# Optimization experiments

Measured on AMD Instinct MI355X. Metric: run time of the kernel, lower is better.

The kernel has to match this reference:

```python
import jax, jax.numpy as jnp
import numpy as np
import math

C = 256
GROUPS = 8
EPS = 1e-5


def setup_inputs() -> dict:
    key = jax.random.key(0)
    ks = jax.random.split(key, 12)
    b, c, h, w = 4, C, 64, 64
    s = 1.0 / math.sqrt(c)
    return {
        "x": jax.random.normal(ks[0], (b, c, h, w), dtype=jnp.float32),
        "gamma": jax.random.normal(ks[1], (c,), dtype=jnp.float32) * 0.1 + 1.0,
        "beta": jax.random.normal(ks[2], (c,), dtype=jnp.float32) * 0.1,
        "wq": jax.random.normal(ks[3], (c, c), dtype=jnp.float32) * s,
        "bq": jnp.zeros((c,), dtype=jnp.float32),
        "wk": jax.random.normal(ks[4], (c, c), dtype=jnp.float32) * s,
        "bk": jnp.zeros((c,), dtype=jnp.float32),
        "wv": jax.random.normal(ks[5], (c, c), dtype=jnp.float32) * s,
        "bv": jnp.zeros((c,), dtype=jnp.float32),
        "wp": jax.random.normal(ks[6], (c, c), dtype=jnp.float32) * s,
        "bp": jnp.zeros((c,), dtype=jnp.float32),
    }


def _group_norm(x, gamma, beta):
    b, c, h, w = x.shape
    xg = x.reshape(b, GROUPS, c // GROUPS, h * w)
    mean = xg.mean(axis=(2, 3), keepdims=True)
    var = xg.var(axis=(2, 3), keepdims=True)
    xn = ((xg - mean) * jax.lax.rsqrt(var + EPS)).reshape(b, c, h, w)
    return xn * gamma[None, :, None, None] + beta[None, :, None, None]


def _conv1x1(x, w, b):
    # 1x1 conv == per-pixel channel GEMM
    return jnp.einsum('oc,bchw->bohw', w, x) + b[None, :, None, None]


def reference(x, gamma, beta, wq, bq, wk, bk, wv, bv, wp, bp):
    b, c, h, w = x.shape
    n = h * w
    xn = _group_norm(x, gamma, beta)
    q = _conv1x1(xn, wq, bq).reshape(b, c, n)  # [b,c,n]
    k = _conv1x1(xn, wk, bk).reshape(b, c, n)
    v = _conv1x1(xn, wv, bv).reshape(b, c, n)
    scale = 1.0 / math.sqrt(c)
    scores = jnp.einsum('bcn,bcm->bnm', q, k) * scale  # [b,n,n]
    attn = jax.nn.softmax(scores, axis=-1)
    out = jnp.einsum('bnm,bcm->bcn', attn, v).reshape(b, c, h, w)
    return _conv1x1(out, wp, bp) + x
```

## Files before the change

### kernel.cpp

```cpp
#include <hip/hip_runtime.h>
#include <hip/hip_bf16.h>
#include <math.h>


#define CCH 256
#define NPIX 4096
#define NB 4
#define NG 8
#define EPS 1e-5f
#define NCHUNK 4

typedef __attribute__((ext_vector_type(8))) short short8;
typedef __attribute__((ext_vector_type(4))) short short4v;
typedef __attribute__((ext_vector_type(4))) float f32x4;
typedef __attribute__((ext_vector_type(16))) float f32x16;
typedef unsigned short ushort_t;
typedef unsigned char u8;

#define GLD16(g, l) __builtin_amdgcn_global_load_lds( \
    (const __attribute__((address_space(1))) unsigned int*)(g), \
    (__attribute__((address_space(3))) unsigned int*)(l), 16, 0, 0)

#define WAITV(n) asm volatile("s_waitcnt vmcnt(" #n ")" ::: "memory")

__device__ inline ushort_t f2bf(float x) {
    union { float f; unsigned u; } c; c.f = x;
    unsigned r = c.u + 0x7FFFu + ((c.u >> 16) & 1u);
    return (ushort_t)(r >> 16);
}
__device__ inline float bf2f(ushort_t h) {
    union { unsigned u; float f; } c; c.u = ((unsigned)h) << 16;
    return c.f;
}
__device__ inline u8 f2fp8(float x) {
    return (u8)(__builtin_amdgcn_cvt_pk_fp8_f32(x, x, 0, false) & 0xff);
}
__device__ inline long mk64(unsigned lo, unsigned hi) {
    return (long)(((unsigned long long)hi << 32) | lo);
}

__global__ __launch_bounds__(256) void gn1w(const float* __restrict__ x,
                                            const float* __restrict__ wq,
                                            const float* __restrict__ wk,
                                            const float* __restrict__ wv,
                                            const float* __restrict__ wp,
                                            float* __restrict__ part,
                                            ushort_t* __restrict__ wbf,
                                            ushort_t* __restrict__ wpbf) {
    int bid = blockIdx.x;
    int t = threadIdx.x;
    if (bid >= 256) {
        int widx = bid - 256;
        int wi = widx >> 6;
        const float* src = wi == 0 ? wq : wi == 1 ? wk : wi == 2 ? wv : wp;
        ushort_t* dst = wi == 3 ? wpbf : wbf + wi * 65536;
        int i = (widx & 63) * 1024 + t * 4;
        float4 v = *(const float4*)(src + i);
        short4v o;
        o[0] = (short)f2bf(v.x); o[1] = (short)f2bf(v.y);
        o[2] = (short)f2bf(v.z); o[3] = (short)f2bf(v.w);
        *(short4v*)(dst + i) = o;
        return;
    }
    int bg = bid >> 3;
    int slice = bid & 7;
    const float* base = x + (size_t)bg * 32 * NPIX + (size_t)slice * 16384;
    float s = 0.f, sq = 0.f;
    for (int i = t; i < 4096; i += 256) {
        float4 v = ((const float4*)base)[i];
        s  += v.x + v.y + v.z + v.w;
        sq += v.x*v.x + v.y*v.y + v.z*v.z + v.w*v.w;
    }
    for (int off = 32; off; off >>= 1) {
        s  += __shfl_down(s,  off);
        sq += __shfl_down(sq, off);
    }
    __shared__ float red[8];
    int wid = t >> 6;
    if ((t & 63) == 0) { red[wid*2] = s; red[wid*2+1] = sq; }
    __syncthreads();
    if (t == 0) {
        float ts = 0.f, tq = 0.f;
        for (int wv2 = 0; wv2 < 4; wv2++) { ts += red[wv2*2]; tq += red[wv2*2+1]; }
        part[bid*2] = ts; part[bid*2+1] = tq;
    }
}

__global__ __launch_bounds__(256) void gn_transpose(const float* __restrict__ x,
                                                    const float* __restrict__ part,
                                                    const float* __restrict__ gamma,
                                                    const float* __restrict__ beta,
                                                    ushort_t* __restrict__ xnT) {
    __shared__ float T[64][69];
    __shared__ float gmean[2], grstd[2];
    int t = threadIdx.x;
    int nBase = blockIdx.x * 64;
    int cBase = blockIdx.y * 64;
    int b = blockIdx.z;
    if (t < 2) {
        int g = (cBase >> 5) + t;
        float s = 0.f, sq = 0.f;
        for (int i = 0; i < 8; i++) {
            s  += part[((b*NG + g)*8 + i)*2];
            sq += part[((b*NG + g)*8 + i)*2 + 1];
        }
        const float inv = 1.f / 131072.f;
        float mean = s * inv;
        float var = sq * inv - mean * mean;
        gmean[t] = mean;
        grstd[t] = rsqrtf(var + EPS);
    }
    __syncthreads();
    const float* xb = x + (size_t)b * CCH * NPIX;
    int n4  = (t & 15) * 4;
    int cc0 = (t >> 4) * 4;
    for (int i = 0; i < 4; i++) {
        int cc = cc0 + i;
        int c = cBase + cc;
        int gi = cc >> 5;
        float ga = gamma[c] * grstd[gi];
        float be = beta[c] - gmean[gi] * ga;
        float4 v = *(const float4*)&xb[(size_t)c * NPIX + nBase + n4];
        T[cc][n4+0] = v.x * ga + be;
        T[cc][n4+1] = v.y * ga + be;
        T[cc][n4+2] = v.z * ga + be;
        T[cc][n4+3] = v.w * ga + be;
    }
    __syncthreads();
    int nn  = t >> 2;
    int ci0 = (t & 3) * 16;
    short8 o0, o1;
    for (int j = 0; j < 8; j++) {
        o0[j] = (short)f2bf(T[ci0 + j][nn]);
        o1[j] = (short)f2bf(T[ci0 + 8 + j][nn]);
    }
    ushort_t* dst = xnT + ((size_t)b * NPIX + nBase + nn) * CCH + cBase + ci0;
    *(short8*)dst = o0;
    *((short8*)dst + 1) = o1;
}

__global__ __launch_bounds__(256, 2) void qkv3(const ushort_t* __restrict__ xnT,
                                               const ushort_t* __restrict__ wbf,
                                               const float* __restrict__ bq,
                                               const float* __restrict__ bk,
                                               const float* __restrict__ bv,
                                               u8* __restrict__ qT,
                                               u8* __restrict__ kT,
                                               u8* __restrict__ vv) {
    __shared__ __align__(16) ushort_t As[2][4096];
    __shared__ __align__(16) ushort_t Bs[2][4096];
    int t = threadIdx.x;
    int w = t >> 6, l = t & 63, quad = l >> 4, l16 = l & 15;
    int z = blockIdx.z;
    const ushort_t* A; const ushort_t* B; int mBase, nBase;
    if (z < 2) { A = xnT; B = wbf + z * 65536; mBase = blockIdx.x * 128; nBase = blockIdx.y * 128; }
    else       { A = wbf + 131072; B = xnT;    mBase = blockIdx.y * 128; nBase = blockIdx.x * 128; }
    int m0 = (w & 1) * 64, n0 = (w >> 1) * 64;

    const f32x4 fz = {0.f, 0.f, 0.f, 0.f};
    f32x4 acc[4][4];
    #pragma unroll
    for (int i = 0; i < 4; i++)
        #pragma unroll
        for (int j = 0; j < 4; j++) acc[i][j] = fz;

    int srow = t >> 2;
    int slc  = (t & 3) ^ ((t >> 2) & 3);
    int sldso = (t >> 6) * 512;

    #pragma unroll
    for (int j = 0; j < 2; j++) {
        int row = 64*j + srow;
        GLD16(A + (size_t)(mBase + row) * 256 + slc * 8, &As[0][j*2048 + sldso]);
        GLD16(B + (size_t)(nBase + row) * 256 + slc * 8, &Bs[0][j*2048 + sldso]);
    }
    int buf = 0;
    for (int kb = 0; kb < 8; kb++) {
        __syncthreads();
        if (kb < 7) {
            #pragma unroll
            for (int j = 0; j < 2; j++) {
                int row = 64*j + srow;
                GLD16(A + (size_t)(mBase + row) * 256 + (kb+1)*32 + slc * 8, &As[buf^1][j*2048 + sldso]);
                GLD16(B + (size_t)(nBase + row) * 256 + (kb+1)*32 + slc * 8, &Bs[buf^1][j*2048 + sldso]);
            }
        }
        short8 af[4], bfr[4];
        #pragma unroll
        for (int mb = 0; mb < 4; mb++)
            af[mb] = *(short8*)&As[buf][(m0 + mb*16 + l16)*32 + ((quad ^ (l16 & 3)) * 8)];
        #pragma unroll
        for (int nb = 0; nb < 4; nb++)
            bfr[nb] = *(short8*)&Bs[buf][(n0 + nb*16 + l16)*32 + ((quad ^ (l16 & 3)) * 8)];
        #pragma unroll
        for (int mb = 0; mb < 4; mb++)
            #pragma unroll
            for (int nb = 0; nb < 4; nb++)
                acc[mb][nb] = __builtin_amdgcn_mfma_f32_16x16x32_bf16(af[mb], bfr[nb], acc[mb][nb], 0, 0, 0);
        buf ^= 1;
    }
    if (z < 2) {
        const float* bias = z ? bk : bq;
        u8* C = z ? kT : qT;
        #pragma unroll
        for (int nb = 0; nb < 4; nb++) {
            int n = nBase + n0 + nb*16 + l16;
            float bb = bias[n];
            #pragma unroll
            for (int mb = 0; mb < 4; mb++)
                #pragma unroll
                for (int r = 0; r < 4; r++) {
                    int m = mBase + m0 + mb*16 + quad*4 + r;
                    C[(size_t)m * 256 + n] = f2fp8(acc[mb][nb][r] + bb);
                }
        }
    } else {
        #pragma unroll
        for (int mb = 0; mb < 4; mb++)
            #pragma unroll
            for (int r = 0; r < 4; r++) {
                int m = mBase + m0 + mb*16 + quad*4 + r;
                float bb = bv[m];
                #pragma unroll
                for (int nb = 0; nb < 4; nb++) {
                    int n = nBase + n0 + nb*16 + l16;
                    vv[((size_t)(n >> 12) * 256 + m) * 4096 + (n & 4095)] = f2fp8(acc[mb][nb][r] + bb);
                }
            }
    }
}

__global__ __launch_bounds__(256, 2) void flash_attn(const u8* __restrict__ qT,
                                                     const u8* __restrict__ kT,
                                                     const u8* __restrict__ vv,
                                                     ushort_t* __restrict__ Op0,
                                                     ushort_t* __restrict__ Op1,
                                                     ushort_t* __restrict__ Op2,
                                                     ushort_t* __restrict__ Op3,
                                                     float* __restrict__ lsum) {
    __shared__ __align__(16) u8 KsAll[3 * 8192];
    __shared__ __align__(16) u8 VsAll[3 * 8192];
    int t = threadIdx.x;
    int w = t >> 6, l = t & 63;
    int l32 = l & 31, hl = l >> 5;
    int flat = blockIdx.x;
    int xcd = flat & 7;
    int ix = flat >> 3;
    int combo = xcd + 8 * (ix >> 5);
    int qg = ix & 31;
    int chunk = combo & 3, b = combo >> 2;
    int qw = qg * 128 + w * 32;

    long qf[16];
    {
        const u8* qrow = qT + ((size_t)b * NPIX + qw + l32) * 256 + hl * 8;
        #pragma unroll
        for (int cb = 0; cb < 16; cb++) qf[cb] = *(const long*)(qrow + cb * 16);
    }

    f32x16 accO[8];
    #pragma unroll
    for (int i = 0; i < 8; i++)
        #pragma unroll
        for (int r = 0; r < 16; r++) accO[i][r] = 0.f;
    float lqa = 0.f;

    const u8* kbase = kT + (size_t)b * NPIX * 256;
    const u8* vbase = vv + (size_t)b * 256 * NPIX;

    const float SC = 0.0625f * 1.44269504089f;
    int mStart = chunk * (NPIX / NCHUNK);
    const int NT = (NPIX / NCHUNK) / 32;

    const u8* kaddr[2];
    const u8* vaddr[2];
    #pragma unroll
    for (int j = 0; j < 2; j++) {
        int n = j * 256 + t;
        int kkv = n >> 4, kcb = (n & 15) ^ (kkv & 7);
        int vc = n >> 1,  vsw = (n & 1) ^ ((vc >> 2) & 1);
        kaddr[j] = kbase + (size_t)(mStart + kkv) * 256 + kcb * 16;
        vaddr[j] = vbase + (size_t)vc * NPIX + mStart + vsw * 16;
    }

    int kO[8];
    #pragma unroll
    for (int c = 0; c < 8; c++) kO[c] = l32 * 256 + ((c ^ (l32 & 7)) * 16) + hl * 8;
    int sw0 = (l32 >> 2) & 1;
    int vO0 = l32 * 32 + (sw0 ^ 0) * 16 + hl * 8;
    int vO1 = l32 * 32 + (sw0 ^ 1) * 16 + hl * 8;

#define LDK(c) (*(const long*)&KsAll[kO[(c) & 7] + (((c) & 8) << 4)])
#define LDV0(m) (*(const long*)&VsAll[vO0 + (m) * 1024])
#define LDV1(m) (*(const long*)&VsAll[vO1 + (m) * 1024])

#define KISSUE(tile, slot) { \
        unsigned koff_ = (unsigned)(tile) * 8192u; \
        _Pragma("unroll") \
        for (int j = 0; j < 2; j++) \
            GLD16(kaddr[j] + koff_, &KsAll[(slot)*8192 + (j*256 + t)*16]); }
#define VISSUE(tile, slot) { \
        unsigned voff_ = (unsigned)(tile) * 32u; \
        _Pragma("unroll") \
        for (int j = 0; j < 2; j++) \
            GLD16(vaddr[j] + voff_, &VsAll[(slot)*8192 + (j*256 + t)*16]); }

#define SOFTMAX_PACK() { \
        float p_[16]; float q0_ = 0.f, q1_ = 0.f; \
        _Pragma("unroll") \
        for (int r = 0; r < 16; r++) { \
            float pe_ = exp2f(fmaf(sTa[r], SC, -5.0f)); \
            pe_ = fminf(pe_, 240.f); \
            p_[r] = pe_; \
            if (r & 1) q1_ += pe_; else q0_ += pe_; \
        } \
        lqa += q0_ + q1_; \
        unsigned pk0_ = (unsigned)__builtin_amdgcn_cvt_pk_fp8_f32(p_[2], p_[3], \
                        __builtin_amdgcn_cvt_pk_fp8_f32(p_[0], p_[1], 0, false), true); \
        unsigned pk1_ = (unsigned)__builtin_amdgcn_cvt_pk_fp8_f32(p_[6], p_[7], \
                        __builtin_amdgcn_cvt_pk_fp8_f32(p_[4], p_[5], 0, false), true); \
        unsigned pk2_ = (unsigned)__builtin_amdgcn_cvt_pk_fp8_f32(p_[10], p_[11], \
                        __builtin_amdgcn_cvt_pk_fp8_f32(p_[8], p_[9], 0, false), true); \
        unsigned pk3_ = (unsigned)__builtin_amdgcn_cvt_pk_fp8_f32(p_[14], p_[15], \
                        __builtin_amdgcn_cvt_pk_fp8_f32(p_[12], p_[13], 0, false), true); \
        asm("v_permlane32_swap_b32 %0, %1" : "+v"(pk0_), "+v"(pk1_)); \
        asm("v_permlane32_swap_b32 %0, %1" : "+v"(pk2_), "+v"(pk3_)); \
        B0 = mk64(pk0_, pk1_); \
        B1 = mk64(pk2_, pk3_); }

#define BURST() { \
        _Pragma("unroll") \
        for (int r = 0; r < 16; r++) sTa[r] = 0.f; \
        _Pragma("unroll") \
        for (int m = 0; m < 8; m++) { \
            sTa = __builtin_amdgcn_mfma_f32_32x32x16_fp8_fp8(LDK(2*m), qf[2*m], sTa, 0, 0, 0); \
            accO[m] = __builtin_amdgcn_mfma_f32_32x32x16_fp8_fp8(LDV0(m), B0, accO[m], 0, 0, 0); \
            sTa = __builtin_amdgcn_mfma_f32_32x32x16_fp8_fp8(LDK(2*m+1), qf[2*m+1], sTa, 0, 0, 0); \
            accO[m] = __builtin_amdgcn_mfma_f32_32x32x16_fp8_fp8(LDV1(m), B1, accO[m], 0, 0, 0); \
        } }

    KISSUE(0, 0);
    VISSUE(0, 0);
    KISSUE(1, 1);
    WAITV(4);
    __builtin_amdgcn_s_barrier();

    f32x16 sTa;
    #pragma unroll
    for (int r = 0; r < 16; r++) sTa[r] = 0.f;
    #pragma unroll
    for (int cb = 0; cb < 16; cb++)
        sTa = __builtin_amdgcn_mfma_f32_32x32x16_fp8_fp8(LDK(cb), qf[cb], sTa, 0, 0, 0);
    long B0, B1;
    SOFTMAX_PACK();

    #pragma unroll
    for (int c = 0; c < 8; c++) kO[c] += 8192;

    int ks_r = 1, ks_w = 2, vs_r = 0, vs_w = 1;
    #pragma unroll 1
    for (int tt = 0; tt < NT - 2; ++tt) {
        KISSUE(tt + 2, ks_w);
        VISSUE(tt + 1, vs_w);
        WAITV(4);
        __builtin_amdgcn_s_barrier();
        __builtin_amdgcn_sched_barrier(0);
        __builtin_amdgcn_s_setprio(1);
        BURST();
        __builtin_amdgcn_s_setprio(0);
        SOFTMAX_PACK();
        int dK = (ks_r == 2) ? -16384 : 8192;
        int dV = (vs_r == 2) ? -16384 : 8192;
        #pragma unroll
        for (int c = 0; c < 8; c++) kO[c] += dK;
        vO0 += dV; vO1 += dV;
        ks_r = ks_r + 1; if (ks_r == 3) ks_r = 0;
        ks_w = ks_w + 1; if (ks_w == 3) ks_w = 0;
        vs_r = vs_r + 1; if (vs_r == 3) vs_r = 0;
        vs_w = vs_w + 1; if (vs_w == 3) vs_w = 0;
    }

    VISSUE(NT - 1, vs_w);
    WAITV(2);
    __builtin_amdgcn_s_barrier();
    __builtin_amdgcn_sched_barrier(0);
    __builtin_amdgcn_s_setprio(1);
    BURST();
    __builtin_amdgcn_s_setprio(0);
    SOFTMAX_PACK();
    {
        int dV = (vs_r == 2) ? -16384 : 8192;
        vO0 += dV; vO1 += dV;
        vs_r = vs_r + 1; if (vs_r == 3) vs_r = 0;
    }

    WAITV(0);
    __builtin_amdgcn_s_barrier();
    {
        __builtin_amdgcn_s_setprio(1);
        #pragma unroll
        for (int m = 0; m < 8; m++) {
            accO[m] = __builtin_amdgcn_mfma_f32_32x32x16_fp8_fp8(LDV0(m), B0, accO[m], 0, 0, 0);
            accO[m] = __builtin_amdgcn_mfma_f32_32x32x16_fp8_fp8(LDV1(m), B1, accO[m], 0, 0, 0);
        }
        __builtin_amdgcn_s_setprio(0);
    }

    {
        float v = lqa + __shfl_xor(lqa, 32);
        if (hl == 0)
            lsum[((size_t)chunk * NB + b) * NPIX + qw + l32] = v;
    }
    ushort_t* op = chunk == 0 ? Op0 : chunk == 1 ? Op1 : chunk == 2 ? Op2 : Op3;
    size_t rowb = ((size_t)b * NPIX + qw + l32) * CCH;
    #pragma unroll
    for (int cblk = 0; cblk < 8; cblk++)
        #pragma unroll
        for (int a = 0; a < 4; a++) {
            short4v o;
            #pragma unroll
            for (int r = 0; r < 4; r++) o[r] = (short)f2bf(accO[cblk][a*4 + r]);
            *(short4v*)&op[rowb + cblk*32 + a*8 + hl*4] = o;
        }
#undef LDK
#undef LDV0
#undef LDV1
#undef KISSUE
#undef VISSUE
#undef SOFTMAX_PACK
#undef BURST
}

__global__ __launch_bounds__(256) void attn_combine(ushort_t* __restrict__ Op0,
                                                    const ushort_t* __restrict__ Op1,
                                                    const ushort_t* __restrict__ Op2,
                                                    const ushort_t* __restrict__ Op3,
                                                    const float* __restrict__ lsum) {
    const size_t BN = (size_t)NB * NPIX;
    size_t base = ((size_t)blockIdx.x * 256 + threadIdx.x) * 4;
    size_t bn = base >> 8;
    float li = 1.f / (lsum[bn] + lsum[BN + bn] + lsum[2*BN + bn] + lsum[3*BN + bn]);
    short4v a0 = *(short4v*)&Op0[base];
    short4v a1 = *(const short4v*)&Op1[base];
    short4v a2 = *(const short4v*)&Op2[base];
    short4v a3 = *(const short4v*)&Op3[base];
    short4v o;
    #pragma unroll
    for (int i = 0; i < 4; i++) {
        float v = (bf2f((ushort_t)a0[i]) + bf2f((ushort_t)a1[i]) +
                   bf2f((ushort_t)a2[i]) + bf2f((ushort_t)a3[i])) * li;
        o[i] = (short)f2bf(v);
    }
    *(short4v*)&Op0[base] = o;
}

__global__ __launch_bounds__(256, 2) void projk(const ushort_t* __restrict__ wpbf,
                                                const ushort_t* __restrict__ aoT,
                                                const float* __restrict__ bp,
                                                const float* __restrict__ x,
                                                float* __restrict__ out) {
    __shared__ __align__(16) ushort_t As[2][4096];
    __shared__ __align__(16) ushort_t Bs[2][4096];
    int t = threadIdx.x;
    int w = t >> 6, l = t & 63, quad = l >> 4, l16 = l & 15;
    int mBase = blockIdx.y * 128, nBase = blockIdx.x * 128;
    int m0 = (w & 1) * 64, n0 = (w >> 1) * 64;

    const f32x4 fz = {0.f, 0.f, 0.f, 0.f};
    f32x4 acc[4][4];
    #pragma unroll
    for (int i = 0; i < 4; i++)
        #pragma unroll
        for (int j = 0; j < 4; j++) acc[i][j] = fz;

    int srow = t >> 2;
    int slc  = (t & 3) ^ ((t >> 2) & 3);
    int sldso = (t >> 6) * 512;

    #pragma unroll
    for (int j = 0; j < 2; j++) {
        int row = 64*j + srow;
        GLD16(wpbf + (size_t)(mBase + row) * 256 + slc * 8, &As[0][j*2048 + sldso]);
        GLD16(aoT  + (size_t)(nBase + row) * 256 + slc * 8, &Bs[0][j*2048 + sldso]);
    }
    int buf = 0;
    for (int kb = 0; kb < 8; kb++) {
        __syncthreads();
        if (kb < 7) {
            #pragma unroll
            for (int j = 0; j < 2; j++) {
                int row = 64*j + srow;
                GLD16(wpbf + (size_t)(mBase + row) * 256 + (kb+1)*32 + slc * 8, &As[buf^1][j*2048 + sldso]);
                GLD16(aoT  + (size_t)(nBase + row) * 256 + (kb+1)*32 + slc * 8, &Bs[buf^1][j*2048 + sldso]);
            }
        }
        short8 af[4], bfr[4];
        #pragma unroll
        for (int mb = 0; mb < 4; mb++)
            af[mb] = *(short8*)&As[buf][(m0 + mb*16 + l16)*32 + ((quad ^ (l16 & 3)) * 8)];
        #pragma unroll
        for (int nb = 0; nb < 4; nb++)
            bfr[nb] = *(short8*)&Bs[buf][(n0 + nb*16 + l16)*32 + ((quad ^ (l16 & 3)) * 8)];
        #pragma unroll
        for (int mb = 0; mb < 4; mb++)
            #pragma unroll
            for (int nb = 0; nb < 4; nb++)
                acc[mb][nb] = __builtin_amdgcn_mfma_f32_16x16x32_bf16(af[mb], bfr[nb], acc[mb][nb], 0, 0, 0);
        buf ^= 1;
    }
    #pragma unroll
    for (int mb = 0; mb < 4; mb++)
        #pragma unroll
        for (int r = 0; r < 4; r++) {
            int m = mBase + m0 + mb*16 + quad*4 + r;
            float bb = bp[m];
            #pragma unroll
            for (int nb = 0; nb < 4; nb++) {
                int n = nBase + n0 + nb*16 + l16;
                size_t idx = ((size_t)(n >> 12) * 256 + m) * 4096 + (n & 4095);
                out[idx] = acc[mb][nb][r] + bb + x[idx];
            }
        }
}

extern "C" void kernel_launch(void* const* d_in, const int* in_sizes, int n_in,
                              void* d_out, int out_size, void* d_ws, size_t ws_size,
                              hipStream_t stream) {
    const float* x     = (const float*)d_in[0];
    const float* gamma = (const float*)d_in[1];
    const float* beta  = (const float*)d_in[2];
    const float* wq    = (const float*)d_in[3];
    const float* bq    = (const float*)d_in[4];
    const float* wk    = (const float*)d_in[5];
    const float* bk    = (const float*)d_in[6];
    const float* wv    = (const float*)d_in[7];
    const float* bv    = (const float*)d_in[8];
    const float* wp    = (const float*)d_in[9];
    const float* bp    = (const float*)d_in[10];
    float* out = (float*)d_out;

    const size_t SZ = (size_t)NB * NPIX * CCH;
    float* part  = (float*)d_ws;
    float* lsum  = part + 512;
    ushort_t* wpbf = (ushort_t*)(lsum + (size_t)NCHUNK * NB * NPIX);
    ushort_t* slot0 = wpbf + 65536;
    ushort_t* Op3 = slot0;
    u8* qT8 = (u8*)(slot0 + SZ);
    u8* kT8 = (u8*)(slot0 + 2*SZ);
    u8* vv8 = (u8*)(slot0 + 3*SZ);
    ushort_t* aoT = slot0 + 4*SZ;
    ushort_t* xnT = (ushort_t*)d_out;
    ushort_t* Op1 = (ushort_t*)d_out;
    ushort_t* Op2 = (ushort_t*)d_out + SZ;
    ushort_t* wbf = (ushort_t*)d_out + SZ;

    gn1w<<<512, 256, 0, stream>>>(x, wq, wk, wv, wp, part, wbf, wpbf);
    gn_transpose<<<dim3(64, 4, 4), 256, 0, stream>>>(x, part, gamma, beta, xnT);
    qkv3<<<dim3(128, 2, 3), 256, 0, stream>>>(xnT, wbf, bq, bk, bv, qT8, kT8, vv8);
    flash_attn<<<dim3(512), 256, 0, stream>>>(qT8, kT8, vv8, aoT, Op1, Op2, Op3, lsum);
    attn_combine<<<(int)(SZ / 1024), 256, 0, stream>>>(aoT, Op1, Op2, Op3, lsum);
    projk<<<dim3(128, 2), 256, 0, stream>>>(wpbf, aoT, bp, x, out);
}
```

Baseline: 196.3 us.

## Use scaled 32x32x64 FP8 MFMA and batch PV over two key tiles

Replaces the 32x32x16 FP8 MFMAs in the flash-attention loop with the MX-scaled 32x32x64 f8f6f4 MFMA, using unit scales. The QK^T step now takes 4 instructions per tile instead of 16. PV is deferred so that one set of 8 wide MFMAs covers two consecutive 32-key tiles, with a permlane swap building the combined P operand. V gets a 4-slot LDS ring to keep two tiles resident, and the XOR swizzles on K and V are dropped. Risks are LDS bank conflicts from the unswizzled 32-byte reads, less interleaving of QK and PV work, and more LDS use, which may affect the 2-blocks-per-CU occupancy.

```diff
diff --git a/kernel.cpp b/kernel.cpp
--- a/kernel.cpp
+++ b/kernel.cpp
@@ -14,6 +14,8 @@
 typedef __attribute__((ext_vector_type(4))) short short4v;
 typedef __attribute__((ext_vector_type(4))) float f32x4;
 typedef __attribute__((ext_vector_type(16))) float f32x16;
+typedef __attribute__((ext_vector_type(4))) int i32x4;
+typedef __attribute__((ext_vector_type(8))) int i32x8;
 typedef unsigned short ushort_t;
 typedef unsigned char u8;
 
@@ -22,6 +24,9 @@
     (__attribute__((address_space(3))) unsigned int*)(l), 16, 0, 0)
 
 #define WAITV(n) asm volatile("s_waitcnt vmcnt(" #n ")" ::: "memory")
+
+#define MXMFMA(A, B, C) __builtin_amdgcn_mfma_scale_f32_32x32x64_f8f6f4( \
+    (A), (B), (C), 0, 0, 0, 0x7F7F7F7F, 0, 0x7F7F7F7F)
 
 __device__ inline ushort_t f2bf(float x) {
     union { float f; unsigned u; } c; c.f = x;
@@ -35,8 +40,13 @@
 __device__ inline u8 f2fp8(float x) {
     return (u8)(__builtin_amdgcn_cvt_pk_fp8_f32(x, x, 0, false) & 0xff);
 }
-__device__ inline long mk64(unsigned lo, unsigned hi) {
-    return (long)(((unsigned long long)hi << 32) | lo);
+__device__ inline i32x8 ld32(const u8* p) {
+    i32x4 a = *(const i32x4*)p;
+    i32x4 b = *(const i32x4*)(p + 16);
+    i32x8 r;
+    r[0] = a[0]; r[1] = a[1]; r[2] = a[2]; r[3] = a[3];
+    r[4] = b[0]; r[5] = b[1]; r[6] = b[2]; r[7] = b[3];
+    return r;
 }
 
 __global__ __launch_bounds__(256) void gn1w(const float* __restrict__ x,
@@ -239,7 +249,7 @@
                                                      ushort_t* __restrict__ Op3,
                                                      float* __restrict__ lsum) {
     __shared__ __align__(16) u8 KsAll[3 * 8192];
-    __shared__ __align__(16) u8 VsAll[3 * 8192];
+    __shared__ __align__(16) u8 VsAll[4 * 8192];
     int t = threadIdx.x;
     int w = t >> 6, l = t & 63;
     int l32 = l & 31, hl = l >> 5;
@@ -251,11 +261,11 @@
     int chunk = combo & 3, b = combo >> 2;
     int qw = qg * 128 + w * 32;
 
-    long qf[16];
+    i32x8 qf4[4];
     {
-        const u8* qrow = qT + ((size_t)b * NPIX + qw + l32) * 256 + hl * 8;
-        #pragma unroll
-        for (int cb = 0; cb < 16; cb++) qf[cb] = *(const long*)(qrow + cb * 16);
+        const u8* qrow = qT + ((size_t)b * NPIX + qw + l32) * 256 + hl * 32;
+        #pragma unroll
+        for (int i = 0; i < 4; i++) qf4[i] = ld32(qrow + i * 64);
     }
 
     f32x16 accO[8];
@@ -277,22 +287,9 @@
     #pragma unroll
     for (int j = 0; j < 2; j++) {
         int n = j * 256 + t;
-        int kkv = n >> 4, kcb = (n & 15) ^ (kkv & 7);
-        int vc = n >> 1,  vsw = (n & 1) ^ ((vc >> 2) & 1);
-        kaddr[j] = kbase + (size_t)(mStart + kkv) * 256 + kcb * 16;
-        vaddr[j] = vbase + (size_t)vc * NPIX + mStart + vsw * 16;
-    }
-
-    int kO[8];
-    #pragma unroll
-    for (int c = 0; c < 8; c++) kO[c] = l32 * 256 + ((c ^ (l32 & 7)) * 16) + hl * 8;
-    int sw0 = (l32 >> 2) & 1;
-    int vO0 = l32 * 32 + (sw0 ^ 0) * 16 + hl * 8;
-    int vO1 = l32 * 32 + (sw0 ^ 1) * 16 + hl * 8;
-
-#define LDK(c) (*(const long*)&KsAll[kO[(c) & 7] + (((c) & 8) << 4)])
-#define LDV0(m) (*(const long*)&VsAll[vO0 + (m) * 1024])
-#define LDV1(m) (*(const long*)&VsAll[vO1 + (m) * 1024])
+        kaddr[j] = kbase + (size_t)(mStart + (n >> 4)) * 256 + (n & 15) * 16;
+        vaddr[j] = vbase + (size_t)(n >> 1) * NPIX + mStart + (n & 1) * 16;
+    }
 
 #define KISSUE(tile, slot) { \
         unsigned koff_ = (unsigned)(tile) * 8192u; \
@@ -305,7 +302,16 @@
         for (int j = 0; j < 2; j++) \
             GLD16(vaddr[j] + voff_, &VsAll[(slot)*8192 + (j*256 + t)*16]); }
 
-#define SOFTMAX_PACK() { \
+#define SCOMPUTE(slot) { \
+        const u8* kb_ = &KsAll[(slot)*8192] + l32*256 + hl*32; \
+        _Pragma("unroll") \
+        for (int r = 0; r < 16; r++) sTa[r] = 0.f; \
+        sTa = MXMFMA(ld32(kb_),       qf4[0], sTa); \
+        sTa = MXMFMA(ld32(kb_ + 64),  qf4[1], sTa); \
+        sTa = MXMFMA(ld32(kb_ + 128), qf4[2], sTa); \
+        sTa = MXMFMA(ld32(kb_ + 192), qf4[3], sTa); }
+
+#define SOFTMAX_PK(dst) { \
         float p_[16]; float q0_ = 0.f, q1_ = 0.f; \
         _Pragma("unroll") \
         for (int r = 0; r < 16; r++) { \
@@ -315,96 +321,72 @@
             if (r & 1) q1_ += pe_; else q0_ += pe_; \
         } \
         lqa += q0_ + q1_; \
-        unsigned pk0_ = (unsigned)__builtin_amdgcn_cvt_pk_fp8_f32(p_[2], p_[3], \
-                        __builtin_amdgcn_cvt_pk_fp8_f32(p_[0], p_[1], 0, false), true); \
-        unsigned pk1_ = (unsigned)__builtin_amdgcn_cvt_pk_fp8_f32(p_[6], p_[7], \
-                        __builtin_amdgcn_cvt_pk_fp8_f32(p_[4], p_[5], 0, false), true); \
-        unsigned pk2_ = (unsigned)__builtin_amdgcn_cvt_pk_fp8_f32(p_[10], p_[11], \
-                        __builtin_amdgcn_cvt_pk_fp8_f32(p_[8], p_[9], 0, false), true); \
-        unsigned pk3_ = (unsigned)__builtin_amdgcn_cvt_pk_fp8_f32(p_[14], p_[15], \
-                        __builtin_amdgcn_cvt_pk_fp8_f32(p_[12], p_[13], 0, false), true); \
-        asm("v_permlane32_swap_b32 %0, %1" : "+v"(pk0_), "+v"(pk1_)); \
-        asm("v_permlane32_swap_b32 %0, %1" : "+v"(pk2_), "+v"(pk3_)); \
-        B0 = mk64(pk0_, pk1_); \
-        B1 = mk64(pk2_, pk3_); }
-
-#define BURST() { \
+        dst[0] = (unsigned)__builtin_amdgcn_cvt_pk_fp8_f32(p_[2], p_[3], \
+                 __builtin_amdgcn_cvt_pk_fp8_f32(p_[0], p_[1], 0, false), true); \
+        dst[1] = (unsigned)__builtin_amdgcn_cvt_pk_fp8_f32(p_[6], p_[7], \
+                 __builtin_amdgcn_cvt_pk_fp8_f32(p_[4], p_[5], 0, false), true); \
+        dst[2] = (unsigned)__builtin_amdgcn_cvt_pk_fp8_f32(p_[10], p_[11], \
+                 __builtin_amdgcn_cvt_pk_fp8_f32(p_[8], p_[9], 0, false), true); \
+        dst[3] = (unsigned)__builtin_amdgcn_cvt_pk_fp8_f32(p_[14], p_[15], \
+                 __builtin_amdgcn_cvt_pk_fp8_f32(p_[12], p_[13], 0, false), true); }
+
+#define OCOMPUTE(slotE, slotO) { \
+        asm("v_permlane32_swap_b32 %0, %1" : "+v"(pkA[0]), "+v"(pkB[0])); \
+        asm("v_permlane32_swap_b32 %0, %1" : "+v"(pkA[1]), "+v"(pkB[1])); \
+        asm("v_permlane32_swap_b32 %0, %1" : "+v"(pkA[2]), "+v"(pkB[2])); \
+        asm("v_permlane32_swap_b32 %0, %1" : "+v"(pkA[3]), "+v"(pkB[3])); \
+        i32x8 pb; \
+        pb[0] = (int)pkA[0]; pb[1] = (int)pkB[0]; \
+        pb[2] = (int)pkA[1]; pb[3] = (int)pkB[1]; \
+        pb[4] = (int)pkA[2]; pb[5] = (int)pkB[2]; \
+        pb[6] = (int)pkA[3]; pb[7] = (int)pkB[3]; \
+        const u8* vb_ = &VsAll[(hl ? (slotO) : (slotE)) * 8192] + l32*32; \
         _Pragma("unroll") \
-        for (int r = 0; r < 16; r++) sTa[r] = 0.f; \
-        _Pragma("unroll") \
-        for (int m = 0; m < 8; m++) { \
-            sTa = __builtin_amdgcn_mfma_f32_32x32x16_fp8_fp8(LDK(2*m), qf[2*m], sTa, 0, 0, 0); \
-            accO[m] = __builtin_amdgcn_mfma_f32_32x32x16_fp8_fp8(LDV0(m), B0, accO[m], 0, 0, 0); \
-            sTa = __builtin_amdgcn_mfma_f32_32x32x16_fp8_fp8(LDK(2*m+1), qf[2*m+1], sTa, 0, 0, 0); \
-            accO[m] = __builtin_amdgcn_mfma_f32_32x32x16_fp8_fp8(LDV1(m), B1, accO[m], 0, 0, 0); \
-        } }
+        for (int cblk = 0; cblk < 8; cblk++) \
+            accO[cblk] = MXMFMA(ld32(vb_ + cblk*1024), pb, accO[cblk]); }
 
     KISSUE(0, 0);
     VISSUE(0, 0);
     KISSUE(1, 1);
-    WAITV(4);
+    WAITV(2);
     __builtin_amdgcn_s_barrier();
 
     f32x16 sTa;
-    #pragma unroll
-    for (int r = 0; r < 16; r++) sTa[r] = 0.f;
-    #pragma unroll
-    for (int cb = 0; cb < 16; cb++)
-        sTa = __builtin_amdgcn_mfma_f32_32x32x16_fp8_fp8(LDK(cb), qf[cb], sTa, 0, 0, 0);
-    long B0, B1;
-    SOFTMAX_PACK();
-
-    #pragma unroll
-    for (int c = 0; c < 8; c++) kO[c] += 8192;
-
-    int ks_r = 1, ks_w = 2, vs_r = 0, vs_w = 1;
+    unsigned pkA[4], pkB[4];
+    SCOMPUTE(0);
+    SOFTMAX_PK(pkA);
+
+    int ks_r = 1, ks_w = 2;
     #pragma unroll 1
     for (int tt = 0; tt < NT - 2; ++tt) {
         KISSUE(tt + 2, ks_w);
-        VISSUE(tt + 1, vs_w);
+        VISSUE(tt + 1, (tt + 1) & 3);
         WAITV(4);
         __builtin_amdgcn_s_barrier();
         __builtin_amdgcn_sched_barrier(0);
         __builtin_amdgcn_s_setprio(1);
-        BURST();
+        if (tt & 1) { OCOMPUTE((tt - 1) & 3, tt & 3); }
+        SCOMPUTE(ks_r);
         __builtin_amdgcn_s_setprio(0);
-        SOFTMAX_PACK();
-        int dK = (ks_r == 2) ? -16384 : 8192;
-        int dV = (vs_r == 2) ? -16384 : 8192;
-        #pragma unroll
-        for (int c = 0; c < 8; c++) kO[c] += dK;
-        vO0 += dV; vO1 += dV;
+        if (tt & 1) { SOFTMAX_PK(pkA); } else { SOFTMAX_PK(pkB); }
         ks_r = ks_r + 1; if (ks_r == 3) ks_r = 0;
         ks_w = ks_w + 1; if (ks_w == 3) ks_w = 0;
-        vs_r = vs_r + 1; if (vs_r == 3) vs_r = 0;
-        vs_w = vs_w + 1; if (vs_w == 3) vs_w = 0;
-    }
-
-    VISSUE(NT - 1, vs_w);
+    }
+
+    VISSUE(NT - 1, (NT - 1) & 3);
     WAITV(2);
     __builtin_amdgcn_s_barrier();
     __builtin_amdgcn_sched_barrier(0);
     __builtin_amdgcn_s_setprio(1);
-    BURST();
+    SCOMPUTE(ks_r);
     __builtin_amdgcn_s_setprio(0);
-    SOFTMAX_PACK();
-    {
-        int dV = (vs_r == 2) ? -16384 : 8192;
-        vO0 += dV; vO1 += dV;
-        vs_r = vs_r + 1; if (vs_r == 3) vs_r = 0;
-    }
+    SOFTMAX_PK(pkB);
 
     WAITV(0);
     __builtin_amdgcn_s_barrier();
-    {
-        __builtin_amdgcn_s_setprio(1);
-        #pragma unroll
-        for (int m = 0; m < 8; m++) {
-            accO[m] = __builtin_amdgcn_mfma_f32_32x32x16_fp8_fp8(LDV0(m), B0, accO[m], 0, 0, 0);
-            accO[m] = __builtin_amdgcn_mfma_f32_32x32x16_fp8_fp8(LDV1(m), B1, accO[m], 0, 0, 0);
-        }
-        __builtin_amdgcn_s_setprio(0);
-    }
+    __builtin_amdgcn_s_setprio(1);
+    OCOMPUTE((NT - 2) & 3, (NT - 1) & 3);
+    __builtin_amdgcn_s_setprio(0);
 
     {
         float v = lqa + __shfl_xor(lqa, 32);
@@ -422,13 +404,11 @@
             for (int r = 0; r < 4; r++) o[r] = (short)f2bf(accO[cblk][a*4 + r]);
             *(short4v*)&op[rowb + cblk*32 + a*8 + hl*4] = o;
         }
-#undef LDK
-#undef LDV0
-#undef LDV1
 #undef KISSUE
 #undef VISSUE
-#undef SOFTMAX_PACK
-#undef BURST
+#undef SCOMPUTE
+#undef SOFTMAX_PK
+#undef OCOMPUTE
 }
 
 __global__ __launch_bounds__(256) void attn_combine(ushort_t* __restrict__ Op0,
```

Measured after the change: 212.1 us. +8.0%, slower.
